# Kernel tuning notes

Hardware: AMD Instinct MI355X
Metric: run time of the kernel (lower is better)

## Reference

```python
import jax, jax.numpy as jnp
import numpy as np

E = 1024          # embed_dim
BUCKET = 16       # bucket_size
TAU = 0.75        # sinkhorn_tau
ITERS = 8         # sinkhorn_iters
SCALE = E ** -0.5


def setup_inputs() -> dict:
    key = jax.random.key(0)
    ks = jax.random.split(key, 12)
    T, S, B = 4096, 4096, 8
    w = 1.0 / np.sqrt(E)  # ~xavier scale
    return {
        "query": jax.random.normal(ks[0], (T, B, E), jnp.float32),
        "key_t": jax.random.normal(ks[1], (S, B, E), jnp.float32),
        "value": jax.random.normal(ks[2], (S, B, E), jnp.float32),
        "key_padding_mask": jnp.zeros((B, S), jnp.bool_),
        "Wq": jax.random.normal(ks[3], (E, E), jnp.float32) * w,
        "bq": jax.random.normal(ks[4], (E,), jnp.float32) * 0.01,
        "Wk": jax.random.normal(ks[5], (E, E), jnp.float32) * w,
        "bk": jax.random.normal(ks[6], (E,), jnp.float32) * 0.01,
        "Wv": jax.random.normal(ks[7], (E, E), jnp.float32) * w,
        "bv": jax.random.normal(ks[8], (E,), jnp.float32) * 0.01,
        "Wo": jax.random.normal(ks[9], (E, E), jnp.float32) * w,
        "bo": jnp.zeros((E,), jnp.float32),
    }


def reference(query, key_t, value, key_padding_mask, Wq, bq, Wk, bk, Wv, bv, Wo, bo):
    # Projections in (T, B, E) layout
    q = query @ Wq.T + bq
    k = key_t @ Wk.T + bk
    v = value @ Wv.T + bv
    # (B, T, E)
    q = jnp.swapaxes(q, 0, 1)
    k = jnp.swapaxes(k, 0, 1)
    v = jnp.swapaxes(v, 0, 1)
    B, T, Ed = q.shape
    S = k.shape[1]
    nb, nkb = T // BUCKET, S // BUCKET  # T,S chosen as exact multiples -> no pad
    # aggregate_buckets: mean-pool q,k; flatten v per bucket
    qb = q.reshape(B, nb, BUCKET, Ed).mean(axis=2)          # (B, nb, E)
    kb = k.reshape(B, nkb, BUCKET, Ed).mean(axis=2)         # (B, nkb, E)
    vb = v.reshape(B, nkb, BUCKET * Ed)                     # (B, nkb, BUCKET*E)
    # key padding mask: bucket is padded iff all positions padded (prod)
    kpm_b = jnp.all(key_padding_mask.reshape(B, nkb, BUCKET), axis=2)  # (B, nkb)
    # energy_fn == 'dot'
    attn = jnp.einsum('bte,bse->bts', qb, kb) * SCALE       # (B, nb, nkb)
    neg_inf = -jnp.finfo(attn.dtype).max
    final_mask = kpm_b[:, None, :] & (~kpm_b)[:, :, None]   # (B, nb, nkb), nb==nkb
    attn = jnp.where(final_mask, neg_inf, attn)
    attn = jnp.where(jnp.swapaxes(final_mask, 1, 2), neg_inf, attn)
    # gumbel_sinkhorn in eval mode (noise_factor=0): log-sinkhorn normalization
    la = attn / TAU
    for _ in range(ITERS):
        la = la - jax.nn.logsumexp(la, axis=-1, keepdims=True)
        la = la - jax.nn.logsumexp(la, axis=-2, keepdims=True)
    p = jnp.exp(la)                                         # (B, nb, nkb)
    # attend over flattened value buckets, then undo bucket aggregation
    out = jnp.einsum('bts,bsf->btf', p, vb)                 # (B, nb, BUCKET*E)
    out = out.reshape(B, nb * BUCKET, Ed)                   # (B, T, E)
    out = jnp.swapaxes(out, 0, 1)                           # (T, B, E)
    return out @ Wo.T + bo
```

## Files before the change

### kernel.cpp

```cpp
#include <hip/hip_runtime.h>


typedef __bf16 bhalf;
typedef __bf16 bh4 __attribute__((ext_vector_type(4)));
typedef __bf16 bh8 __attribute__((ext_vector_type(8)));
typedef float f32x4 __attribute__((ext_vector_type(4)));

__device__ __forceinline__ void async16(const bhalf* g, bhalf* l) {
    __builtin_amdgcn_global_load_lds(
        (const __attribute__((address_space(1))) unsigned int*)g,
        (__attribute__((address_space(3))) unsigned int*)l,
        16, 0, 0);
}

__device__ __forceinline__ void f2b_body(const float* in, bhalf* out, int idx) {
    const float4* p = (const float4*)in + (size_t)idx * 2;
    float4 x = p[0], y = p[1];
    bh8 o;
    o[0] = (bhalf)x.x; o[1] = (bhalf)x.y; o[2] = (bhalf)x.z; o[3] = (bhalf)x.w;
    o[4] = (bhalf)y.x; o[5] = (bhalf)y.y; o[6] = (bhalf)y.z; o[7] = (bhalf)y.w;
    *(bh8*)(out + (size_t)idx * 8) = o;
}

__global__ void f2b_kernel(const float* __restrict__ in, bhalf* __restrict__ out, int n8) {
    int idx = blockIdx.x * 256 + threadIdx.x;
    if (idx < n8) f2b_body(in, out, idx);
}

__global__ void f2b4_kernel(const float* __restrict__ a, const float* __restrict__ b,
                            const float* __restrict__ c, const float* __restrict__ d,
                            bhalf* __restrict__ out) {
    const float* srcs[4] = {a, b, c, d};
    int idx = blockIdx.x * 256 + threadIdx.x;
    f2b_body(srcs[blockIdx.y], out + (size_t)blockIdx.y * 1048576, idx);
}

__global__ void pool2_kernel(const float* __restrict__ q, const float* __restrict__ k,
                             bhalf* __restrict__ oq, bhalf* __restrict__ ok) {
    const float* in = blockIdx.y ? k : q;
    bhalf* out = blockIdx.y ? ok : oq;
    int row = blockIdx.x;
    int b = row >> 8, tb = row & 255;
    int e = threadIdx.x * 4;
    const float* base = in + ((size_t)(tb * 16) * 8 + b) * 1024 + e;
    float sx = 0.f, sy = 0.f, sz = 0.f, sw = 0.f;
#pragma unroll
    for (int i = 0; i < 16; ++i) {
        float4 v = *(const float4*)(base + (size_t)i * 8192);
        sx += v.x; sy += v.y; sz += v.z; sw += v.w;
    }
    bh4 o;
    o[0] = (bhalf)(sx * 0.0625f);
    o[1] = (bhalf)(sy * 0.0625f);
    o[2] = (bhalf)(sz * 0.0625f);
    o[3] = (bhalf)(sw * 0.0625f);
    *(bh4*)(out + (size_t)row * 1024 + e) = o;
}

__global__ __launch_bounds__(256) void gemm_nt(
    const bhalf* __restrict__ A, const bhalf* __restrict__ B,
    void* __restrict__ Cv, const float* __restrict__ bias, const float* __restrict__ bias2,
    int lda, int ldb, long ldc, int K,
    float alpha, int outBf16, int swz,
    long zsA, long zsB, long zsC, unsigned zmaskA)
{
    __shared__ bhalf As[128 * 64];
    __shared__ bhalf Bs[128 * 64];
    unsigned z = blockIdx.z;
    A += (size_t)(z & zmaskA) * zsA;
    B += (size_t)z * zsB;
    if (z == 1 && bias2) bias = bias2;
    long coff = (long)z * zsC;
    int bx = blockIdx.x, by = blockIdx.y;
    if (swz) {
        int linear = by * 8 + bx;
        int xcd = linear & 7, idx = linear >> 3;
        bx = idx & 7;
        by = xcd * ((int)gridDim.y >> 3) + (idx >> 3);
    }
    int m0 = by * 128, n0 = bx * 128;
    int tid = threadIdx.x;
    int w = tid >> 6, lane = tid & 63;
    int quad = lane >> 4, l16 = lane & 15;
    int wm = (w & 1) * 64, wn = (w >> 1) * 64;
    int srow = lane >> 3;
    int sg = (lane & 7) ^ srow;

    f32x4 acc[4][4] = {};

    for (int k0 = 0; k0 < K; k0 += 64) {
#pragma unroll
        for (int j = 0; j < 4; ++j) {
            int blk = j * 4 + w;
            int r = blk * 8 + srow;
            async16(A + (size_t)(m0 + r) * lda + (k0 + sg * 8), &As[blk * 512]);
            async16(B + (size_t)(n0 + r) * ldb + (k0 + sg * 8), &Bs[blk * 512]);
        }
        __syncthreads();
#pragma unroll
        for (int kk = 0; kk < 2; ++kk) {
            bh8 fa[4], fb[4];
            int gsw = (((kk << 2) + quad) ^ (l16 & 7)) * 8;
#pragma unroll
            for (int i = 0; i < 4; ++i) {
                fa[i] = *(const bh8*)&As[(wm + i * 16 + l16) * 64 + gsw];
                fb[i] = *(const bh8*)&Bs[(wn + i * 16 + l16) * 64 + gsw];
            }
#pragma unroll
            for (int i = 0; i < 4; ++i)
#pragma unroll
                for (int j = 0; j < 4; ++j)
                    acc[i][j] = __builtin_amdgcn_mfma_f32_16x16x32_bf16(
                        fa[i], fb[j], acc[i][j], 0, 0, 0);
        }
        __syncthreads();
    }

#pragma unroll
    for (int i = 0; i < 4; ++i) {
        int row = m0 + wm + i * 16 + quad * 4;
#pragma unroll
        for (int j = 0; j < 4; ++j) {
            int col = n0 + wn + j * 16 + l16;
            float bb = bias ? bias[col] : 0.f;
#pragma unroll
            for (int r2 = 0; r2 < 4; ++r2) {
                float v = alpha * acc[i][j][r2] + bb;
                long off = coff + (long)(row + r2) * ldc + col;
                if (outBf16) ((bhalf*)Cv)[off] = (bhalf)v;
                else         ((float*)Cv)[off] = v;
            }
        }
    }
}

__device__ __forceinline__ void stage256(const bhalf* __restrict__ A,
                                         const bhalf* __restrict__ B,
                                         bhalf* as, bhalf* bs,
                                         int m0, int n0, int lda, int ldb,
                                         int k0, int w, int lane)
{
    int r8 = lane >> 3;
    int colb = k0 + (((lane & 7) ^ r8) << 3);
    const bhalf* ap = A + (size_t)(m0 + w * 8 + r8) * lda + colb;
    const bhalf* bp = B + (size_t)(n0 + w * 8 + r8) * ldb + colb;
    bhalf* asw = as + w * 512;
    bhalf* bsw = bs + w * 512;
#pragma unroll
    for (int s = 0; s < 4; ++s) {
        async16(ap + (size_t)(s * 64) * lda, asw + s * 4096);
        async16(bp + (size_t)(s * 64) * ldb, bsw + s * 4096);
    }
}

__device__ __forceinline__ void compute256(const bhalf* as, const bhalf* bs,
                                           int wr, int wc, int quad, int l16,
                                           f32x4 (&acc)[8][4])
{
#pragma unroll
    for (int kk = 0; kk < 2; ++kk) {
        bh8 fa[8], fb[4];
        int gsw = (((kk << 2) + quad) ^ (l16 & 7)) << 3;
#pragma unroll
        for (int i = 0; i < 8; ++i)
            fa[i] = *(const bh8*)&as[(wr * 128 + i * 16 + l16) * 64 + gsw];
#pragma unroll
        for (int j = 0; j < 4; ++j)
            fb[j] = *(const bh8*)&bs[(wc * 64 + j * 16 + l16) * 64 + gsw];
        __builtin_amdgcn_s_setprio(1);
#pragma unroll
        for (int i = 0; i < 8; ++i)
#pragma unroll
            for (int j = 0; j < 4; ++j)
                acc[i][j] = __builtin_amdgcn_mfma_f32_16x16x32_bf16(
                    fa[i], fb[j], acc[i][j], 0, 0, 0);
        __builtin_amdgcn_s_setprio(0);
    }
}

__global__ __launch_bounds__(512, 2) void gemm256(
    const bhalf* __restrict__ A, const bhalf* __restrict__ B,
    void* __restrict__ Cv, const float* __restrict__ bias,
    int K, int outBf16)
{
    __shared__ __align__(16) bhalf As[2][16384];
    __shared__ __align__(16) bhalf Bs[2][16384];

    int nx = (int)gridDim.x;
    int linear = blockIdx.y * nx + blockIdx.x;
    int xcd = linear & 7, idx = linear >> 3;
    int bx = idx % nx;
    int by = xcd * ((int)gridDim.y >> 3) + idx / nx;
    int m0 = by << 8, n0 = bx << 8;

    int tid = threadIdx.x;
    int w = tid >> 6, lane = tid & 63;
    int quad = lane >> 4, l16 = lane & 15;
    int wr = w & 1, wc = w >> 1;
    const int lda = K, ldb = K;

    f32x4 acc[8][4] = {};
    int nt = K >> 6;

    stage256(A, B, As[0], Bs[0], m0, n0, lda, ldb, 0, w, lane);
    for (int t = 0; t < nt - 1; ++t) {
        stage256(A, B, As[(t + 1) & 1], Bs[(t + 1) & 1], m0, n0, lda, ldb,
                 (t + 1) << 6, w, lane);
        asm volatile("s_waitcnt vmcnt(8)" ::: "memory");
        asm volatile("s_barrier" ::: "memory");
        compute256(As[t & 1], Bs[t & 1], wr, wc, quad, l16, acc);
        asm volatile("s_barrier" ::: "memory");
    }
    asm volatile("s_waitcnt vmcnt(0)" ::: "memory");
    asm volatile("s_barrier" ::: "memory");
    compute256(As[(nt - 1) & 1], Bs[(nt - 1) & 1], wr, wc, quad, l16, acc);

    const long ldc = 1024;
#pragma unroll
    for (int i = 0; i < 8; ++i) {
        int row = m0 + wr * 128 + i * 16 + quad * 4;
#pragma unroll
        for (int j = 0; j < 4; ++j) {
            int col = n0 + wc * 64 + j * 16 + l16;
            float bb = bias[col];
#pragma unroll
            for (int r2 = 0; r2 < 4; ++r2) {
                float v = acc[i][j][r2] + bb;
                long off = (long)(row + r2) * ldc + col;
                if (outBf16) ((bhalf*)Cv)[off] = (bhalf)v;
                else         ((float*)Cv)[off] = v;
            }
        }
    }
}

__global__ __launch_bounds__(1024) void sinkhorn_kernel(
    const float* __restrict__ la_in, bhalf* __restrict__ p_out)
{
    int b = blockIdx.x;
    const float* A = la_in + (size_t)b * 65536;
    int tid = threadIdx.x;
    int br = tid >> 5, bc = tid & 31;
    int r0 = br * 8, c0 = bc * 8;
    float a[8][8];
#pragma unroll
    for (int r = 0; r < 8; ++r) {
        float4 v0 = *(const float4*)(A + (size_t)(r0 + r) * 256 + c0);
        float4 v1 = *(const float4*)(A + (size_t)(r0 + r) * 256 + c0 + 4);
        a[r][0] = v0.x; a[r][1] = v0.y; a[r][2] = v0.z; a[r][3] = v0.w;
        a[r][4] = v1.x; a[r][5] = v1.y; a[r][6] = v1.z; a[r][7] = v1.w;
    }
    __shared__ float lm[16][256];
    __shared__ float ls[16][256];

    for (int it = 0; it < 8; ++it) {
#pragma unroll
        for (int r = 0; r < 8; ++r) {
            float m = a[r][0];
#pragma unroll
            for (int c = 1; c < 8; ++c) m = fmaxf(m, a[r][c]);
#pragma unroll
            for (int d = 1; d < 32; d <<= 1) m = fmaxf(m, __shfl_xor(m, d, 64));
            float s = 0.f;
#pragma unroll
            for (int c = 0; c < 8; ++c) s += __expf(a[r][c] - m);
#pragma unroll
            for (int d = 1; d < 32; d <<= 1) s += __shfl_xor(s, d, 64);
            float lse = m + __logf(s);
#pragma unroll
            for (int c = 0; c < 8; ++c) a[r][c] -= lse;
        }
        __syncthreads();
#pragma unroll
        for (int c = 0; c < 8; ++c) {
            float m = a[0][c];
#pragma unroll
            for (int r = 1; r < 8; ++r) m = fmaxf(m, a[r][c]);
            float s = 0.f;
#pragma unroll
            for (int r = 0; r < 8; ++r) s += __expf(a[r][c] - m);
            float mo = __shfl_xor(m, 32, 64);
            float so = __shfl_xor(s, 32, 64);
            float M2 = fmaxf(m, mo);
            float S2 = s * __expf(m - M2) + so * __expf(mo - M2);
            if ((br & 1) == 0) { lm[br >> 1][c0 + c] = M2; ls[br >> 1][c0 + c] = S2; }
        }
        __syncthreads();
        if (tid < 256) {
            int col = tid;
            float M = lm[0][col];
#pragma unroll
            for (int j = 1; j < 16; ++j) M = fmaxf(M, lm[j][col]);
            float S = 0.f;
#pragma unroll
            for (int j = 0; j < 16; ++j) S += ls[j][col] * __expf(lm[j][col] - M);
            lm[0][col] = M + __logf(S);
        }
        __syncthreads();
#pragma unroll
        for (int c = 0; c < 8; ++c) {
            float lse = lm[0][c0 + c];
#pragma unroll
            for (int r = 0; r < 8; ++r) a[r][c] -= lse;
        }
    }
#pragma unroll
    for (int r = 0; r < 8; ++r) {
        bh8 o;
#pragma unroll
        for (int c = 0; c < 8; ++c) o[c] = (bhalf)__expf(a[r][c]);
        *(bh8*)(p_out + (size_t)b * 65536 + (size_t)(r0 + r) * 256 + c0) = o;
    }
}

__global__ void transpose_v_kernel(const bhalf* __restrict__ vp, bhalf* __restrict__ vT) {
    int z = blockIdx.x;
    int i = z >> 3, b = z & 7;
    int e0 = blockIdx.y * 64, s0 = blockIdx.z * 64;
    __shared__ bhalf t[64][72];
    for (int g = threadIdx.x; g < 512; g += 256) {
        int r = g >> 3, gc = g & 7;
        size_t row = ((size_t)(s0 + r) * 16 + i) * 8 + b;
        *(uint4*)&t[r][gc * 8] = *(const uint4*)(vp + row * 1024 + e0 + gc * 8);
    }
    __syncthreads();
    for (int g = threadIdx.x; g < 512; g += 256) {
        int er = g >> 3, gc = g & 7;
        bh8 o;
#pragma unroll
        for (int j = 0; j < 8; ++j) o[j] = t[gc * 8 + j][er];
        *(bh8*)(vT + (size_t)z * 262144 + (size_t)(e0 + er) * 256 + (s0 + gc * 8)) = o;
    }
}

extern "C" void kernel_launch(void* const* d_in, const int* in_sizes, int n_in,
                              void* d_out, int out_size, void* d_ws, size_t ws_size,
                              hipStream_t stream) {
    const float* query = (const float*)d_in[0];
    const float* key_t = (const float*)d_in[1];
    const float* value = (const float*)d_in[2];
    const float* Wq = (const float*)d_in[4];
    const float* bq = (const float*)d_in[5];
    const float* Wk = (const float*)d_in[6];
    const float* bk = (const float*)d_in[7];
    const float* Wv = (const float*)d_in[8];
    const float* bv = (const float*)d_in[9];
    const float* Wo = (const float*)d_in[10];
    const float* bo = (const float*)d_in[11];

    char* ws = (char*)d_ws;
    bhalf* val_bf = (bhalf*)(ws);
    bhalf* vT     = val_bf;
    bhalf* vproj  = (bhalf*)(ws + 67108864);
    bhalf* outp   = vproj;
    bhalf* Wq_b   = (bhalf*)(ws + 134217728);
    bhalf* Wk_b   = Wq_b + 1048576;
    bhalf* Wv_b   = Wk_b + 1048576;
    bhalf* Wo_b   = Wv_b + 1048576;
    bhalf* qp     = Wo_b + 1048576;
    bhalf* kp     = qp + 2097152;
    bhalf* qbp    = kp + 2097152;
    bhalf* kbp    = qbp + 2097152;
    float* la     = (float*)(kbp + 2097152);
    bhalf* p_bf   = (bhalf*)(la + 524288);

    const float SCALE_TAU = (1.0f / 32.0f) / 0.75f;
    const unsigned ALLZ = 0xffffffffu;

    f2b4_kernel<<<dim3(512, 4), 256, 0, stream>>>(Wq, Wk, Wv, Wo, Wq_b);
    f2b_kernel<<<16384, 256, 0, stream>>>(value, val_bf, 4194304);

    pool2_kernel<<<dim3(2048, 2), 256, 0, stream>>>(query, key_t, qp, kp);

    gemm_nt<<<dim3(8, 16, 2), 256, 0, stream>>>(qp, Wq_b, qbp, bq, bk,
        1024, 1024, 1024, 1024, 1.0f, 1, 0, 2097152, 1048576, 2097152, ALLZ);

    gemm_nt<<<dim3(2, 2, 8), 256, 0, stream>>>(qbp, kbp, la, nullptr, nullptr,
        1024, 1024, 256, 1024, SCALE_TAU, 0, 0, 262144, 262144, 65536, ALLZ);

    sinkhorn_kernel<<<8, 1024, 0, stream>>>(la, p_bf);

    gemm256<<<dim3(4, 128), 512, 0, stream>>>(val_bf, Wv_b, vproj, bv, 1024, 1);

    transpose_v_kernel<<<dim3(128, 16, 4), 256, 0, stream>>>(vproj, vT);

    gemm_nt<<<dim3(8, 2, 128), 256, 0, stream>>>(p_bf, vT, outp, nullptr, nullptr,
        256, 256, 131072, 256, 1.0f, 1, 0, 65536, 262144, 1024, 7u);

    gemm256<<<dim3(4, 128), 512, 0, stream>>>(outp, Wo_b, (float*)d_out, bo, 1024, 0);
}
```

Before: 770.5 us.

## Split gemm256 k-tile into four phases interleaving async loads with MFMA

Restructures the 256x256 GEMM main loop so each k-tile is processed in four phases of 2x4 MFMA blocks. The global-to-LDS prefetch of the next tile is split into quarters issued between those phases. Fragment loads are pinned ahead of the MFMAs with sched_barrier. The goal is finer overlap of memory traffic with matrix math and lower register pressure, at the cost of extra barriers per tile.

Result: no change. 772.7 us (+0.3%).

```diff
diff --git a/kernel.cpp b/kernel.cpp
--- a/kernel.cpp
+++ b/kernel.cpp
@@ -134,47 +134,23 @@
     }
 }
 
-__device__ __forceinline__ void stage256(const bhalf* __restrict__ A,
-                                         const bhalf* __restrict__ B,
-                                         bhalf* as, bhalf* bs,
-                                         int m0, int n0, int lda, int ldb,
-                                         int k0, int w, int lane)
+__device__ __forceinline__ void stage_half(const bhalf* __restrict__ A,
+                                           const bhalf* __restrict__ B,
+                                           bhalf* as, bhalf* bs,
+                                           int m0, int n0, int ld,
+                                           int k0, int h, int w, int lane)
 {
     int r8 = lane >> 3;
     int colb = k0 + (((lane & 7) ^ r8) << 3);
-    const bhalf* ap = A + (size_t)(m0 + w * 8 + r8) * lda + colb;
-    const bhalf* bp = B + (size_t)(n0 + w * 8 + r8) * ldb + colb;
-    bhalf* asw = as + w * 512;
-    bhalf* bsw = bs + w * 512;
-#pragma unroll
-    for (int s = 0; s < 4; ++s) {
-        async16(ap + (size_t)(s * 64) * lda, asw + s * 4096);
-        async16(bp + (size_t)(s * 64) * ldb, bsw + s * 4096);
-    }
-}
-
-__device__ __forceinline__ void compute256(const bhalf* as, const bhalf* bs,
-                                           int wr, int wc, int quad, int l16,
-                                           f32x4 (&acc)[8][4])
-{
-#pragma unroll
-    for (int kk = 0; kk < 2; ++kk) {
-        bh8 fa[8], fb[4];
-        int gsw = (((kk << 2) + quad) ^ (l16 & 7)) << 3;
-#pragma unroll
-        for (int i = 0; i < 8; ++i)
-            fa[i] = *(const bh8*)&as[(wr * 128 + i * 16 + l16) * 64 + gsw];
-#pragma unroll
-        for (int j = 0; j < 4; ++j)
-            fb[j] = *(const bh8*)&bs[(wc * 64 + j * 16 + l16) * 64 + gsw];
-        __builtin_amdgcn_s_setprio(1);
-#pragma unroll
-        for (int i = 0; i < 8; ++i)
-#pragma unroll
-            for (int j = 0; j < 4; ++j)
-                acc[i][j] = __builtin_amdgcn_mfma_f32_16x16x32_bf16(
-                    fa[i], fb[j], acc[i][j], 0, 0, 0);
-        __builtin_amdgcn_s_setprio(0);
+    const bhalf* M = (h < 2) ? A : B;
+    bhalf* L = (h < 2) ? as : bs;
+    int row0 = (h < 2) ? m0 : n0;
+    int hh = (h & 1) * 2;
+#pragma unroll
+    for (int ss = 0; ss < 2; ++ss) {
+        int s = hh + ss;
+        async16(M + (size_t)(row0 + s * 64 + w * 8 + r8) * ld + colb,
+                L + w * 512 + s * 4096);
     }
 }
 
@@ -197,23 +173,94 @@
     int w = tid >> 6, lane = tid & 63;
     int quad = lane >> 4, l16 = lane & 15;
     int wr = w & 1, wc = w >> 1;
-    const int lda = K, ldb = K;
+    const int ld = K;
 
     f32x4 acc[8][4] = {};
     int nt = K >> 6;
 
-    stage256(A, B, As[0], Bs[0], m0, n0, lda, ldb, 0, w, lane);
-    for (int t = 0; t < nt - 1; ++t) {
-        stage256(A, B, As[(t + 1) & 1], Bs[(t + 1) & 1], m0, n0, lda, ldb,
-                 (t + 1) << 6, w, lane);
-        asm volatile("s_waitcnt vmcnt(8)" ::: "memory");
+    int gswB = (quad ^ (l16 & 7)) << 3;
+    int gswB1 = ((4 + quad) ^ (l16 & 7)) << 3;
+    int arow0 = (wr * 128 + l16) * 64;
+    int brow0 = (wc * 64 + l16) * 64;
+
+#pragma unroll
+    for (int h = 0; h < 4; ++h)
+        stage_half(A, B, As[0], Bs[0], m0, n0, ld, 0, h, w, lane);
+
+    int cur = 0;
+    for (int t = 0; t < nt; ++t) {
+        const bhalf* as = As[cur];
+        const bhalf* bs = Bs[cur];
+        bhalf* asn = As[cur ^ 1];
+        bhalf* bsn = Bs[cur ^ 1];
+        bool pre = (t + 1 < nt);
+        int kn = (t + 1) << 6;
+
+        bh8 fb[4][2];
+
+        if (pre) {
+            stage_half(A, B, asn, bsn, m0, n0, ld, kn, 0, w, lane);
+            asm volatile("s_waitcnt vmcnt(2)" ::: "memory");
+        } else {
+            asm volatile("s_waitcnt vmcnt(0)" ::: "memory");
+        }
         asm volatile("s_barrier" ::: "memory");
-        compute256(As[t & 1], Bs[t & 1], wr, wc, quad, l16, acc);
+        {
+            bh8 fa[2][2];
+#pragma unroll
+            for (int j = 0; j < 4; ++j) {
+                fb[j][0] = *(const bh8*)&bs[brow0 + j * 16 * 64 + gswB];
+                fb[j][1] = *(const bh8*)&bs[brow0 + j * 16 * 64 + gswB1];
+            }
+#pragma unroll
+            for (int i2 = 0; i2 < 2; ++i2) {
+                fa[i2][0] = *(const bh8*)&as[arow0 + i2 * 16 * 64 + gswB];
+                fa[i2][1] = *(const bh8*)&as[arow0 + i2 * 16 * 64 + gswB1];
+            }
+            asm volatile("s_waitcnt lgkmcnt(0)" ::: "memory");
+            __builtin_amdgcn_sched_barrier(0);
+            __builtin_amdgcn_s_setprio(1);
+#pragma unroll
+            for (int i2 = 0; i2 < 2; ++i2)
+#pragma unroll
+                for (int j = 0; j < 4; ++j) {
+                    acc[i2][j] = __builtin_amdgcn_mfma_f32_16x16x32_bf16(
+                        fa[i2][0], fb[j][0], acc[i2][j], 0, 0, 0);
+                    acc[i2][j] = __builtin_amdgcn_mfma_f32_16x16x32_bf16(
+                        fa[i2][1], fb[j][1], acc[i2][j], 0, 0, 0);
+                }
+            __builtin_amdgcn_s_setprio(0);
+        }
         asm volatile("s_barrier" ::: "memory");
-    }
-    asm volatile("s_waitcnt vmcnt(0)" ::: "memory");
-    asm volatile("s_barrier" ::: "memory");
-    compute256(As[(nt - 1) & 1], Bs[(nt - 1) & 1], wr, wc, quad, l16, acc);
+
+#pragma unroll
+        for (int p = 1; p < 4; ++p) {
+            bh8 fa[2][2];
+#pragma unroll
+            for (int i2 = 0; i2 < 2; ++i2) {
+                int ar = arow0 + (p * 2 + i2) * 16 * 64;
+                fa[i2][0] = *(const bh8*)&as[ar + gswB];
+                fa[i2][1] = *(const bh8*)&as[ar + gswB1];
+            }
+            if (pre) stage_half(A, B, asn, bsn, m0, n0, ld, kn, p, w, lane);
+            asm volatile("s_barrier" ::: "memory");
+            asm volatile("s_waitcnt lgkmcnt(0)" ::: "memory");
+            __builtin_amdgcn_sched_barrier(0);
+            __builtin_amdgcn_s_setprio(1);
+#pragma unroll
+            for (int i2 = 0; i2 < 2; ++i2)
+#pragma unroll
+                for (int j = 0; j < 4; ++j) {
+                    acc[p * 2 + i2][j] = __builtin_amdgcn_mfma_f32_16x16x32_bf16(
+                        fa[i2][0], fb[j][0], acc[p * 2 + i2][j], 0, 0, 0);
+                    acc[p * 2 + i2][j] = __builtin_amdgcn_mfma_f32_16x16x32_bf16(
+                        fa[i2][1], fb[j][1], acc[p * 2 + i2][j], 0, 0, 0);
+                }
+            __builtin_amdgcn_s_setprio(0);
+            asm volatile("s_barrier" ::: "memory");
+        }
+        cur ^= 1;
+    }
 
     const long ldc = 1024;
 #pragma unroll
```

## Fold V projection into output projection via precomputed Wo·Wv product

Applied to the files above, without the earlier changes.

The V projection is moved past the linear sinkhorn attention: a combined weight U = Wo·Wv is precomputed once, and the bias term bv becomes a rank-1 correction (row sums of P times Wo·bv) added in the final GEMM epilogue. This removes the full-size value projection GEMM and the separate fp32-to-bf16 value conversion. Raw values are converted and transposed directly, and the sinkhorn kernel also emits row sums. Precision changes slightly because attention now runs on unprojected bf16 values and U is rounded to bf16.

Result: faster. 689.2 us (-10.5%).

```diff
diff --git a/kernel.cpp b/kernel.cpp
--- a/kernel.cpp
+++ b/kernel.cpp
@@ -22,17 +22,51 @@
     *(bh8*)(out + (size_t)idx * 8) = o;
 }
 
-__global__ void f2b_kernel(const float* __restrict__ in, bhalf* __restrict__ out, int n8) {
-    int idx = blockIdx.x * 256 + threadIdx.x;
-    if (idx < n8) f2b_body(in, out, idx);
-}
-
 __global__ void f2b4_kernel(const float* __restrict__ a, const float* __restrict__ b,
                             const float* __restrict__ c, const float* __restrict__ d,
                             bhalf* __restrict__ out) {
     const float* srcs[4] = {a, b, c, d};
     int idx = blockIdx.x * 256 + threadIdx.x;
     f2b_body(srcs[blockIdx.y], out + (size_t)blockIdx.y * 1048576, idx);
+}
+
+__global__ void wvT_kernel(const float* __restrict__ W, bhalf* __restrict__ WT) {
+    int f0 = blockIdx.x * 64, g0 = blockIdx.y * 64;
+    __shared__ bhalf t[64][72];
+    for (int g = threadIdx.x; g < 512; g += 256) {
+        int r = g >> 3, gc = g & 7;
+        const float* src = W + (size_t)(f0 + r) * 1024 + g0 + gc * 8;
+        float4 x = *(const float4*)src, y = *(const float4*)(src + 4);
+        bh8 o;
+        o[0] = (bhalf)x.x; o[1] = (bhalf)x.y; o[2] = (bhalf)x.z; o[3] = (bhalf)x.w;
+        o[4] = (bhalf)y.x; o[5] = (bhalf)y.y; o[6] = (bhalf)y.z; o[7] = (bhalf)y.w;
+        *(bh8*)&t[r][gc * 8] = o;
+    }
+    __syncthreads();
+    for (int g = threadIdx.x; g < 512; g += 256) {
+        int gr = g >> 3, gc = g & 7;
+        bh8 o;
+#pragma unroll
+        for (int j = 0; j < 8; ++j) o[j] = t[gc * 8 + j][gr];
+        *(bh8*)(WT + (size_t)(g0 + gr) * 1024 + f0 + gc * 8) = o;
+    }
+}
+
+__global__ void c0_kernel(const float* __restrict__ Wo, const float* __restrict__ bv,
+                          float* __restrict__ c0) {
+    int n = blockIdx.x * 4 + (threadIdx.x >> 6);
+    int lane = threadIdx.x & 63;
+    const float* row = Wo + (size_t)n * 1024;
+    float s = 0.f;
+#pragma unroll
+    for (int f = lane * 4; f < 1024; f += 256) {
+        float4 w = *(const float4*)(row + f);
+        float4 x = *(const float4*)(bv + f);
+        s += w.x * x.x + w.y * x.y + w.z * x.z + w.w * x.w;
+    }
+#pragma unroll
+    for (int d = 1; d < 64; d <<= 1) s += __shfl_xor(s, d, 64);
+    if (lane == 0) c0[n] = s;
 }
 
 __global__ void pool2_kernel(const float* __restrict__ q, const float* __restrict__ k,
@@ -181,6 +215,7 @@
 __global__ __launch_bounds__(512, 2) void gemm256(
     const bhalf* __restrict__ A, const bhalf* __restrict__ B,
     void* __restrict__ Cv, const float* __restrict__ bias,
+    const float* __restrict__ c0p, const float* __restrict__ rsp,
     int K, int outBf16)
 {
     __shared__ __align__(16) bhalf As[2][16384];
@@ -219,13 +254,23 @@
 #pragma unroll
     for (int i = 0; i < 8; ++i) {
         int row = m0 + wr * 128 + i * 16 + quad * 4;
+        float rsv[4];
+        if (rsp) {
+#pragma unroll
+            for (int r2 = 0; r2 < 4; ++r2) {
+                int rr = row + r2;
+                rsv[r2] = rsp[(rr & 7) * 256 + (rr >> 7)];
+            }
+        }
 #pragma unroll
         for (int j = 0; j < 4; ++j) {
             int col = n0 + wc * 64 + j * 16 + l16;
             float bb = bias[col];
+            float cc = c0p ? c0p[col] : 0.f;
 #pragma unroll
             for (int r2 = 0; r2 < 4; ++r2) {
                 float v = acc[i][j][r2] + bb;
+                if (rsp) v += rsv[r2] * cc;
                 long off = (long)(row + r2) * ldc + col;
                 if (outBf16) ((bhalf*)Cv)[off] = (bhalf)v;
                 else         ((float*)Cv)[off] = v;
@@ -235,7 +280,8 @@
 }
 
 __global__ __launch_bounds__(1024) void sinkhorn_kernel(
-    const float* __restrict__ la_in, bhalf* __restrict__ p_out)
+    const float* __restrict__ la_in, bhalf* __restrict__ p_out,
+    float* __restrict__ rs_out)
 {
     int b = blockIdx.x;
     const float* A = la_in + (size_t)b * 65536;
@@ -307,13 +353,22 @@
 #pragma unroll
     for (int r = 0; r < 8; ++r) {
         bh8 o;
-#pragma unroll
-        for (int c = 0; c < 8; ++c) o[c] = (bhalf)__expf(a[r][c]);
+        float rowacc = 0.f;
+#pragma unroll
+        for (int c = 0; c < 8; ++c) {
+            float e = __expf(a[r][c]);
+            o[c] = (bhalf)e;
+            rowacc += e;
+        }
+#pragma unroll
+        for (int d = 1; d < 32; d <<= 1) rowacc += __shfl_xor(rowacc, d, 64);
+        if (bc == 0) rs_out[b * 256 + r0 + r] = rowacc;
         *(bh8*)(p_out + (size_t)b * 65536 + (size_t)(r0 + r) * 256 + c0) = o;
     }
 }
 
-__global__ void transpose_v_kernel(const bhalf* __restrict__ vp, bhalf* __restrict__ vT) {
+__global__ void transpose_vf32_kernel(const float* __restrict__ vp,
+                                      bhalf* __restrict__ vT) {
     int z = blockIdx.x;
     int i = z >> 3, b = z & 7;
     int e0 = blockIdx.y * 64, s0 = blockIdx.z * 64;
@@ -321,7 +376,12 @@
     for (int g = threadIdx.x; g < 512; g += 256) {
         int r = g >> 3, gc = g & 7;
         size_t row = ((size_t)(s0 + r) * 16 + i) * 8 + b;
-        *(uint4*)&t[r][gc * 8] = *(const uint4*)(vp + row * 1024 + e0 + gc * 8);
+        const float* src = vp + row * 1024 + e0 + gc * 8;
+        float4 x = *(const float4*)src, y = *(const float4*)(src + 4);
+        bh8 o;
+        o[0] = (bhalf)x.x; o[1] = (bhalf)x.y; o[2] = (bhalf)x.z; o[3] = (bhalf)x.w;
+        o[4] = (bhalf)y.x; o[5] = (bhalf)y.y; o[6] = (bhalf)y.z; o[7] = (bhalf)y.w;
+        *(bh8*)&t[r][gc * 8] = o;
     }
     __syncthreads();
     for (int g = threadIdx.x; g < 512; g += 256) {
@@ -349,26 +409,30 @@
     const float* bo = (const float*)d_in[11];
 
     char* ws = (char*)d_ws;
-    bhalf* val_bf = (bhalf*)(ws);
-    bhalf* vT     = val_bf;
-    bhalf* vproj  = (bhalf*)(ws + 67108864);
-    bhalf* outp   = vproj;
+    bhalf* vT     = (bhalf*)(ws);
+    bhalf* outp   = (bhalf*)(ws + 67108864);
     bhalf* Wq_b   = (bhalf*)(ws + 134217728);
     bhalf* Wk_b   = Wq_b + 1048576;
-    bhalf* Wv_b   = Wk_b + 1048576;
-    bhalf* Wo_b   = Wv_b + 1048576;
+    bhalf* WvT_b  = Wk_b + 1048576;
+    bhalf* Wo_b   = WvT_b + 1048576;
     bhalf* qp     = Wo_b + 1048576;
     bhalf* kp     = qp + 2097152;
     bhalf* qbp    = kp + 2097152;
     bhalf* kbp    = qbp + 2097152;
     float* la     = (float*)(kbp + 2097152);
     bhalf* p_bf   = (bhalf*)(la + 524288);
+    bhalf* U_b    = p_bf + 524288;
+    float* c0     = (float*)(U_b + 1048576);
+    float* rs     = c0 + 1024;
 
     const float SCALE_TAU = (1.0f / 32.0f) / 0.75f;
     const unsigned ALLZ = 0xffffffffu;
 
     f2b4_kernel<<<dim3(512, 4), 256, 0, stream>>>(Wq, Wk, Wv, Wo, Wq_b);
-    f2b_kernel<<<16384, 256, 0, stream>>>(value, val_bf, 4194304);
+    wvT_kernel<<<dim3(16, 16), 256, 0, stream>>>(Wv, WvT_b);
+    c0_kernel<<<256, 256, 0, stream>>>(Wo, bv, c0);
+    gemm_nt<<<dim3(8, 8, 1), 256, 0, stream>>>(Wo_b, WvT_b, U_b, nullptr, nullptr,
+        1024, 1024, 1024, 1024, 1.0f, 1, 0, 0, 0, 0, 0u);
 
     pool2_kernel<<<dim3(2048, 2), 256, 0, stream>>>(query, key_t, qp, kp);
 
@@ -378,14 +442,13 @@
     gemm_nt<<<dim3(2, 2, 8), 256, 0, stream>>>(qbp, kbp, la, nullptr, nullptr,
         1024, 1024, 256, 1024, SCALE_TAU, 0, 0, 262144, 262144, 65536, ALLZ);
 
-    sinkhorn_kernel<<<8, 1024, 0, stream>>>(la, p_bf);
-
-    gemm256<<<dim3(4, 128), 512, 0, stream>>>(val_bf, Wv_b, vproj, bv, 1024, 1);
-
-    transpose_v_kernel<<<dim3(128, 16, 4), 256, 0, stream>>>(vproj, vT);
+    sinkhorn_kernel<<<8, 1024, 0, stream>>>(la, p_bf, rs);
+
+    transpose_vf32_kernel<<<dim3(128, 16, 4), 256, 0, stream>>>(value, vT);
 
     gemm_nt<<<dim3(8, 2, 128), 256, 0, stream>>>(p_bf, vT, outp, nullptr, nullptr,
         256, 256, 131072, 256, 1.0f, 1, 0, 65536, 262144, 1024, 7u);
 
-    gemm256<<<dim3(4, 128), 512, 0, stream>>>(outp, Wo_b, (float*)d_out, bo, 1024, 0);
-}
+    gemm256<<<dim3(4, 128), 512, 0, stream>>>(outp, U_b, (float*)d_out, bo,
+        c0, rs, 1024, 0);
+}
```
